# Kernel tuning notes

Hardware: AMD Instinct MI355X
Metric: run time of the kernel (lower is better)

Reference implementation:

```python
import jax, jax.numpy as jnp
import numpy as np

B, T, H, D = 16, 128, 512, 256
VIN, VOUT = 32000, 32000


def _lstm_cell(xt, h, c, W, U, b):
    # Keras LSTMCell gate order: i, f, g(candidate), o
    z = xt @ W + h @ U + b  # [B, 4H]
    i, f, g, o = jnp.split(z, 4, axis=-1)
    c = jax.nn.sigmoid(f) * c + jax.nn.sigmoid(i) * jnp.tanh(g)
    h = jax.nn.sigmoid(o) * jnp.tanh(c)
    return h, c


def _lstm_seq(x, W, U, b, h0, c0):
    # x: [B,T,Din] -> seq [B,T,H], final (h,c)
    def step(carry, xt):
        h, c = _lstm_cell(xt, carry[0], carry[1], W, U, b)
        return (h, c), h
    (hT, cT), seq = jax.lax.scan(step, (h0, c0), jnp.swapaxes(x, 0, 1))
    return jnp.swapaxes(seq, 0, 1), hT, cT


def setup_inputs() -> dict:
    key = jax.random.key(0)
    ks = jax.random.split(key, 16)
    s = lambda fan: 1.0 / np.sqrt(fan).astype(np.float32)
    f32 = jnp.float32
    return {
        "tokens": jax.random.randint(ks[0], (B, T), 0, VIN + 1),
        "emb": jax.random.normal(ks[1], (VIN + 1, D), f32) * 0.02,
        "W1": jax.random.normal(ks[2], (D, 4 * H), f32) * s(D),
        "U1": jax.random.normal(ks[3], (H, 4 * H), f32) * s(H),
        "b1": jnp.zeros((4 * H,), f32),
        "W2": jax.random.normal(ks[4], (H, 4 * H), f32) * s(H),
        "U2": jax.random.normal(ks[5], (H, 4 * H), f32) * s(H),
        "b2": jnp.zeros((4 * H,), f32),
        "Wd1": jax.random.normal(ks[6], (H, 4 * H), f32) * s(H),
        "Ud1": jax.random.normal(ks[7], (H, 4 * H), f32) * s(H),
        "bd1": jnp.zeros((4 * H,), f32),
        "Wd2": jax.random.normal(ks[8], (H, 4 * H), f32) * s(H),
        "Ud2": jax.random.normal(ks[9], (H, 4 * H), f32) * s(H),
        "bd2": jnp.zeros((4 * H,), f32),
        "Wo": jax.random.normal(ks[10], (2 * H, VOUT + 1), f32) * s(2 * H),
        "bo": jnp.zeros((VOUT + 1,), f32),
    }


def reference(tokens, emb, W1, U1, b1, W2, U2, b2, Wd1, Ud1, bd1, Wd2, Ud2, bd2, Wo, bo):
    x = emb[tokens]  # [B,T,D]
    zeros = jnp.zeros((tokens.shape[0], H), x.dtype)
    seq1, h1, c1 = _lstm_seq(x, W1, U1, b1, zeros, zeros)
    # layer-2 encoder initialized with layer-1 final states (as in source)
    seq2, h2, c2 = _lstm_seq(seq1, W2, U2, b2, h1, c1)

    def dec_step(carry, xt):
        (hA, cA), (hB, cB) = carry
        hA, cA = _lstm_cell(xt, hA, cA, Wd1, Ud1, bd1)
        hB, cB = _lstm_cell(hA, hB, cB, Wd2, Ud2, bd2)
        # global Luong dot attention over full encoder-2 sequence
        score = jax.nn.softmax(jnp.einsum('bsh,bh->bs', seq2, hB), axis=-1)
        ctx = jnp.einsum('bsh,bs->bh', seq2, score)
        out = jnp.concatenate([hB, ctx], axis=-1)  # [B, 2H]
        return ((hA, cA), (hB, cB)), out

    # decoder input is the encoder-2 sequence, time-major
    _, outs = jax.lax.scan(dec_step, ((h1, c1), (h2, c2)), jnp.swapaxes(seq2, 0, 1))
    dec = jnp.swapaxes(outs, 0, 1)  # [B,T,2H]
    logits = dec @ Wo + bo  # [B,T,VOUT+1]
    return jax.nn.softmax(logits, axis=-1)
```

## Files before the change

### kernel.cpp

```cpp
#include <hip/hip_runtime.h>
#include <hip/hip_bf16.h>
#include <math.h>

#define Bq   16
#define Tq   128
#define Hq   512
#define Dq   256
#define G4H  2048
#define MR   2048
#define VO   32001
#define NPAD 32128
#define NBLK 32
#define BH   (Bq * Hq)
#define HP64 4096

typedef unsigned int u32;
typedef unsigned long long u64;
typedef __attribute__((ext_vector_type(4))) float f32x4;
typedef __attribute__((ext_vector_type(8))) short bfrag;
typedef __attribute__((ext_vector_type(4))) float facc;

__device__ __forceinline__ float bf2f(short s) {
  union { unsigned u; float f; } v; v.u = ((unsigned)(unsigned short)s) << 16; return v.f;
}
__device__ __forceinline__ short f2bf(float f) {
  union { float f; unsigned u; } v; v.f = f;
  unsigned r = (v.u + 0x7fffu + ((v.u >> 16) & 1u)) >> 16;
  return (short)r;
}
__device__ __forceinline__ float sigm(float x) { return 1.0f / (1.0f + expf(-x)); }

__device__ __forceinline__ void ic_store64(u64* p, u64 v) {
  __hip_atomic_store(p, v, __ATOMIC_RELAXED, __HIP_MEMORY_SCOPE_AGENT);
}
__device__ __forceinline__ u64 ic_load64(const u64* p) {
  return __hip_atomic_load(p, __ATOMIC_RELAXED, __HIP_MEMORY_SCOPE_AGENT);
}

__device__ __forceinline__ void barsig(u32* flags, u32 ph) {
  asm volatile("s_waitcnt vmcnt(0)" ::: "memory");
  __syncthreads();
  if (threadIdx.x == 0)
    __hip_atomic_store(&flags[blockIdx.x * 32], ph, __ATOMIC_RELAXED, __HIP_MEMORY_SCOPE_AGENT);
}
__device__ __forceinline__ void barwait(u32* flags, u32 ph) {
  if (threadIdx.x < NBLK) {
    while (__hip_atomic_load(&flags[threadIdx.x * 32], __ATOMIC_RELAXED, __HIP_MEMORY_SCOPE_AGENT) < ph)
      __builtin_amdgcn_s_sleep(1);
  }
  __syncthreads();
}

__device__ __forceinline__ void* swz(void* plane, int row, int byteoff) {
  return (void*)((char*)plane + row * 1040 + (byteoff ^ ((row & 7) << 4)));
}

__global__ __launch_bounds__(256) void k_transcvt(const float* __restrict__ in,
                                                  short* __restrict__ out,
                                                  int R, int N, int perm) {
  __shared__ float tile[32][33];
  int nb = blockIdx.x * 32, rb = blockIdx.y * 32;
  int tx = threadIdx.x & 31, ty = threadIdx.x >> 5;
  for (int i = 0; i < 4; ++i) {
    int r = rb + ty + i * 8;
    int n = nb + tx;
    tile[ty + i * 8][tx] = (n < N) ? in[(size_t)r * N + n] : 0.0f;
  }
  __syncthreads();
  for (int i = 0; i < 4; ++i) {
    int n = nb + ty + i * 8;
    int orow = perm ? (((n & 511) << 2) | (n >> 9)) : n;
    out[(size_t)orow * R + rb + tx] = f2bf(tile[tx][ty + i * 8]);
  }
}

__global__ __launch_bounds__(256) void k_cvt(const float* __restrict__ in,
                                             short* __restrict__ out, int n) {
  int i = (blockIdx.x * 256 + threadIdx.x) * 4;
  if (i + 3 < n) {
    f32x4 v = *(const f32x4*)(in + i);
    short4 o;
    o.x = f2bf(v[0]); o.y = f2bf(v[1]); o.z = f2bf(v[2]); o.w = f2bf(v[3]);
    *(short4*)(out + i) = o;
  }
}

__global__ __launch_bounds__(256) void k_gather(const int* __restrict__ tokens,
                                                const float* __restrict__ emb,
                                                short* __restrict__ xbf) {
  int row = blockIdx.x;
  int t = row >> 4, b = row & 15;
  int tok = tokens[b * Tq + t];
  xbf[(size_t)row * Dq + threadIdx.x] = f2bf(emb[(size_t)tok * Dq + threadIdx.x]);
}

__global__ __launch_bounds__(256) void k_gemm(const short* __restrict__ A,
                                              const short* __restrict__ BT,
                                              float* __restrict__ C,
                                              const float* __restrict__ bias,
                                              int M, int Nreal, int K, int ldc,
                                              int permb) {
  __shared__ short lA[128 * 64];
  __shared__ short lB[128 * 64];
  const int tid = threadIdx.x;
  const int wave = tid >> 6, lane = tid & 63;
  const int l15 = lane & 15, l4 = lane >> 4;
  const int m0 = blockIdx.y * 128, n0 = blockIdx.x * 128;
  const int wm = (wave >> 1) * 64, wn = (wave & 1) * 64;
  facc acc[4][4] = {};

  for (int k0 = 0; k0 < K; k0 += 64) {
    __syncthreads();
    for (int i = 0; i < 4; ++i) {
      int c = i * 256 + wave * 64 + lane;
      int r = c >> 3, q = c & 7;
      int qs = q ^ (r & 7);
      const short* ga = A + (size_t)(m0 + r) * K + k0 + qs * 8;
      const short* gb = BT + (size_t)(n0 + r) * K + k0 + qs * 8;
      short* la = lA + (size_t)(i * 256 + wave * 64) * 8;
      short* lb = lB + (size_t)(i * 256 + wave * 64) * 8;
      __builtin_amdgcn_global_load_lds((const __attribute__((address_space(1))) u32*)ga,
                                       (__attribute__((address_space(3))) u32*)la, 16, 0, 0);
      __builtin_amdgcn_global_load_lds((const __attribute__((address_space(1))) u32*)gb,
                                       (__attribute__((address_space(3))) u32*)lb, 16, 0, 0);
    }
    __syncthreads();
    for (int ks = 0; ks < 2; ++ks) {
      bfrag a[4], b[4];
      for (int mi = 0; mi < 4; ++mi) {
        int r = wm + mi * 16 + l15;
        int qs = (ks * 4 + l4) ^ (r & 7);
        a[mi] = *(const bfrag*)&lA[r * 64 + qs * 8];
      }
      for (int ni = 0; ni < 4; ++ni) {
        int r = wn + ni * 16 + l15;
        int qs = (ks * 4 + l4) ^ (r & 7);
        b[ni] = *(const bfrag*)&lB[r * 64 + qs * 8];
      }
      for (int mi = 0; mi < 4; ++mi)
        for (int ni = 0; ni < 4; ++ni)
          acc[mi][ni] = __builtin_amdgcn_mfma_f32_16x16x32_bf16(a[mi], b[ni], acc[mi][ni], 0, 0, 0);
    }
  }
  for (int ni = 0; ni < 4; ++ni) {
    int col = n0 + wn + ni * 16 + l15;
    if (col >= Nreal) continue;
    int bcol = permb ? (((col & 3) << 9) | (col >> 2)) : col;
    float bs = bias ? bias[bcol] : 0.0f;
    for (int mi = 0; mi < 4; ++mi) {
      int rb = m0 + wm + mi * 16 + l4 * 4;
      facc v = acc[mi][ni];
      C[(size_t)(rb + 0) * ldc + col] = v[0] + bs;
      C[(size_t)(rb + 1) * ldc + col] = v[1] + bs;
      C[(size_t)(rb + 2) * ldc + col] = v[2] + bs;
      C[(size_t)(rb + 3) * ldc + col] = v[3] + bs;
    }
  }
}


__global__ __launch_bounds__(512) void k_rec(const float* __restrict__ XW,
                                             const short* __restrict__ UT,
                                             const float* __restrict__ hinit,
                                             const float* __restrict__ cinit,
                                             u64* __restrict__ hbuf,
                                             float* __restrict__ hfin,
                                             float* __restrict__ cfin,
                                             short* __restrict__ seq_bf,
                                             float* __restrict__ seq_f32,
                                             u32* flags, int dry) {
  __shared__ short lh[2][16][520];
  __shared__ float zt[8][16][20];
  const int tid = threadIdx.x;
  const int wv = tid >> 6, lane = tid & 63;
  const int l15 = lane & 15, l4 = lane >> 4;
  const int kh = wv >> 2;
  const int gw = blockIdx.x * 4 + (wv & 3);
  const int bb = lane >> 2, jj = lane & 3;
  const int hidx = gw * 4 + jj;

  bfrag ur[8];
  {
    const short* ub = UT + (size_t)(gw * 16 + l15) * Hq + kh * 256 + l4 * 8;
    #pragma unroll
    for (int ks = 0; ks < 8; ++ks) ur[ks] = *(const bfrag*)&ub[ks * 32];
  }
  float c = 0.0f;
  if (wv < 4) {
    c = cinit ? cinit[bb * Hq + hidx] : 0.0f;
    float hv = hinit ? hinit[bb * Hq + hidx] : 0.0f;
    int hi_ = (int)(unsigned short)f2bf(hv);
    int lo_ = (int)(unsigned short)f2bf(hv - bf2f((short)hi_));
    int hi2 = __shfl_xor(hi_, 1), lo2 = __shfl_xor(lo_, 1);
    if ((jj & 1) == 0) {
      u64 v = (u64)((u32)hi_ | ((u32)hi2 << 16)) | ((u64)((u32)lo_ | ((u32)lo2 << 16)) << 32);
      ic_store64(&hbuf[(bb * Hq + hidx) >> 1], v);
    }
  }
  u32 ph = 0;
  for (int d = 0; d < dry; ++d) { ++ph; barsig(flags, ph); barwait(flags, ph); }
  ++ph; barsig(flags, ph); barwait(flags, ph);

  for (int s = 0; s < Tq; ++s) {
    f32x4 xg = {};
    if (wv < 4) xg = *(const f32x4*)&XW[(size_t)(s * Bq + bb) * G4H + hidx * 4];
    const u64* hsrc = hbuf + (size_t)(s & 1) * HP64;
    #pragma unroll
    for (int it = 0; it < 8; ++it) {
      int i = it * 512 + tid;
      u64 v = ic_load64(&hsrc[i]);
      int b = i >> 8, bo = (i & 255) * 4;
      *(u32*)swz(&lh[0][0][0], b, bo) = (u32)v;
      *(u32*)swz(&lh[1][0][0], b, bo) = (u32)(v >> 32);
    }
    __syncthreads();
    facc a0 = {}, a1 = {};
    #pragma unroll
    for (int ks = 0; ks < 8; ++ks) {
      int bo = kh * 512 + ks * 64 + l4 * 16;
      bfrag ah = *(const bfrag*)swz(&lh[0][0][0], l15, bo);
      bfrag al = *(const bfrag*)swz(&lh[1][0][0], l15, bo);
      a0 = __builtin_amdgcn_mfma_f32_16x16x32_bf16(ah, ur[ks], a0, 0, 0, 0);
      a1 = __builtin_amdgcn_mfma_f32_16x16x32_bf16(al, ur[ks], a1, 0, 0, 0);
    }
    a0 += a1;
    *(f32x4*)&zt[wv][l15][l4 * 4] = a0;
    __syncthreads();
    float hN = 0.0f; int hi_ = 0;
    if (wv < 4) {
      float zi = zt[wv][4 * jj + 0][bb] + zt[wv + 4][4 * jj + 0][bb] + xg[0];
      float zf = zt[wv][4 * jj + 1][bb] + zt[wv + 4][4 * jj + 1][bb] + xg[1];
      float zg = zt[wv][4 * jj + 2][bb] + zt[wv + 4][4 * jj + 2][bb] + xg[2];
      float zo = zt[wv][4 * jj + 3][bb] + zt[wv + 4][4 * jj + 3][bb] + xg[3];
      c = sigm(zf) * c + sigm(zi) * tanhf(zg);
      hN = sigm(zo) * tanhf(c);
      hi_ = (int)(unsigned short)f2bf(hN);
      int lo_ = (int)(unsigned short)f2bf(hN - bf2f((short)hi_));
      int hi2 = __shfl_xor(hi_, 1), lo2 = __shfl_xor(lo_, 1);
      if (s < Tq - 1 && (jj & 1) == 0) {
        u64 v = (u64)((u32)hi_ | ((u32)hi2 << 16)) | ((u64)((u32)lo_ | ((u32)lo2 << 16)) << 32);
        ic_store64(&hbuf[(size_t)((s + 1) & 1) * HP64 + ((bb * Hq + hidx) >> 1)], v);
      }
    }
    if (s < Tq - 1) {
      ++ph; barsig(flags, ph);
      if (wv < 4) {
        seq_bf[(size_t)(s * Bq + bb) * Hq + hidx] = (short)hi_;
        if (seq_f32) seq_f32[(size_t)(s * Bq + bb) * Hq + hidx] = hN;
      }
      barwait(flags, ph);
    } else if (wv < 4) {
      seq_bf[(size_t)(s * Bq + bb) * Hq + hidx] = (short)hi_;
      if (seq_f32) seq_f32[(size_t)(s * Bq + bb) * Hq + hidx] = hN;
      hfin[bb * Hq + hidx] = hN;
      cfin[bb * Hq + hidx] = c;
    }
  }
}

__global__ __launch_bounds__(512) void k_dec2(const float* __restrict__ XW,
                                              const short* __restrict__ U1T,
                                              const short* __restrict__ W2T,
                                              const short* __restrict__ U2T,
                                              const float* __restrict__ bd2,
                                              const float* __restrict__ h1f, const float* __restrict__ c1f,
                                              const float* __restrict__ h2f, const float* __restrict__ c2f,
                                              u64* __restrict__ hAbuf, u64* __restrict__ hBbuf,
                                              float* __restrict__ hBseq, float* __restrict__ decb,
                                              u32* flags) {
  __shared__ short lA[2][16][520];
  __shared__ short lB[2][16][520];
  __shared__ float ztA[8][16][20];
  __shared__ float ztB[8][16][20];
  const int tid = threadIdx.x;
  const int wv = tid >> 6, lane = tid & 63;
  const int l15 = lane & 15, l4 = lane >> 4;
  const int kh = wv >> 2;
  const int gw = blockIdx.x * 4 + (wv & 3);
  const int bb = lane >> 2, jj = lane & 3;
  const int hidx = gw * 4 + jj;

  bfrag u1r[8], w2r[8], u2r[8];
  {
    size_t ro = (size_t)(gw * 16 + l15) * Hq + kh * 256 + l4 * 8;
    #pragma unroll
    for (int ks = 0; ks < 8; ++ks) {
      u1r[ks] = *(const bfrag*)&U1T[ro + ks * 32];
      w2r[ks] = *(const bfrag*)&W2T[ro + ks * 32];
      u2r[ks] = *(const bfrag*)&U2T[ro + ks * 32];
    }
  }
  float cc = 0.0f, bdi = 0, bdf = 0, bdg = 0, bdo = 0;
  {
    const float* cf = (wv < 4) ? c1f : c2f;
    const float* hf = (wv < 4) ? h1f : h2f;
    cc = cf[bb * Hq + hidx];
    float hv = hf[bb * Hq + hidx];
    int hi_ = (int)(unsigned short)f2bf(hv);
    int lo_ = (int)(unsigned short)f2bf(hv - bf2f((short)hi_));
    int hi2 = __shfl_xor(hi_, 1), lo2 = __shfl_xor(lo_, 1);
    if ((jj & 1) == 0) {
      u64 v = (u64)((u32)hi_ | ((u32)hi2 << 16)) | ((u64)((u32)lo_ | ((u32)lo2 << 16)) << 32);
      u64* hb = (wv < 4) ? hAbuf : hBbuf;
      int pi = (bb * Hq + hidx) >> 1;
      ic_store64(&hb[pi], v);
      ic_store64(&hb[HP64 + pi], v);
    }
    if (wv >= 4) {
      bdi = bd2[hidx]; bdf = bd2[Hq + hidx];
      bdg = bd2[2 * Hq + hidx]; bdo = bd2[3 * Hq + hidx];
    }
  }
  u32 ph = 1;
  barsig(flags, ph); barwait(flags, ph);

  for (int p = 0; p <= Tq; ++p) {
    f32x4 xg = {};
    if (wv < 4 && p < Tq) xg = *(const f32x4*)&XW[(size_t)(p * Bq + bb) * G4H + hidx * 4];
    const u64* asrc = hAbuf + (size_t)(p & 1) * HP64;
    const u64* bsrc = hBbuf + (size_t)(p & 1) * HP64;
    #pragma unroll
    for (int it = 0; it < 8; ++it) {
      int i = it * 512 + tid;
      u64 va = ic_load64(&asrc[i]);
      u64 vb = ic_load64(&bsrc[i]);
      int b = i >> 8, bo = (i & 255) * 4;
      *(u32*)swz(&lA[0][0][0], b, bo) = (u32)va;
      *(u32*)swz(&lA[1][0][0], b, bo) = (u32)(va >> 32);
      *(u32*)swz(&lB[0][0][0], b, bo) = (u32)vb;
      *(u32*)swz(&lB[1][0][0], b, bo) = (u32)(vb >> 32);
    }
    __syncthreads();

    facc a0 = {}, a1 = {}, b0 = {}, b1 = {}, b2 = {}, b3 = {};
    #pragma unroll
    for (int ks = 0; ks < 8; ++ks) {
      int bo = kh * 512 + ks * 64 + l4 * 16;
      bfrag ah = *(const bfrag*)swz(&lA[0][0][0], l15, bo);
      bfrag al = *(const bfrag*)swz(&lA[1][0][0], l15, bo);
      if (p < Tq) {
        a0 = __builtin_amdgcn_mfma_f32_16x16x32_bf16(ah, u1r[ks], a0, 0, 0, 0);
        a1 = __builtin_amdgcn_mfma_f32_16x16x32_bf16(al, u1r[ks], a1, 0, 0, 0);
      }
      if (p >= 1) {
        bfrag hh = *(const bfrag*)swz(&lB[0][0][0], l15, bo);
        bfrag hl = *(const bfrag*)swz(&lB[1][0][0], l15, bo);
        b0 = __builtin_amdgcn_mfma_f32_16x16x32_bf16(ah, w2r[ks], b0, 0, 0, 0);
        b1 = __builtin_amdgcn_mfma_f32_16x16x32_bf16(al, w2r[ks], b1, 0, 0, 0);
        b2 = __builtin_amdgcn_mfma_f32_16x16x32_bf16(hh, u2r[ks], b2, 0, 0, 0);
        b3 = __builtin_amdgcn_mfma_f32_16x16x32_bf16(hl, u2r[ks], b3, 0, 0, 0);
      }
    }
    if (p < Tq) { a0 += a1; *(f32x4*)&ztA[wv][l15][l4 * 4] = a0; }
    if (p >= 1) { b0 += b1; b0 += b2; b0 += b3; *(f32x4*)&ztB[wv][l15][l4 * 4] = b0; }
    __syncthreads();

    float hNB = 0.0f;
    if (wv < 4 && p < Tq) {
      float zi = ztA[wv][4 * jj + 0][bb] + ztA[wv + 4][4 * jj + 0][bb] + xg[0];
      float zf = ztA[wv][4 * jj + 1][bb] + ztA[wv + 4][4 * jj + 1][bb] + xg[1];
      float zg = ztA[wv][4 * jj + 2][bb] + ztA[wv + 4][4 * jj + 2][bb] + xg[2];
      float zo = ztA[wv][4 * jj + 3][bb] + ztA[wv + 4][4 * jj + 3][bb] + xg[3];
      cc = sigm(zf) * cc + sigm(zi) * tanhf(zg);
      float hN = sigm(zo) * tanhf(cc);
      int hi_ = (int)(unsigned short)f2bf(hN);
      int lo_ = (int)(unsigned short)f2bf(hN - bf2f((short)hi_));
      int hi2 = __shfl_xor(hi_, 1), lo2 = __shfl_xor(lo_, 1);
      if ((jj & 1) == 0) {
        u64 v = (u64)((u32)hi_ | ((u32)hi2 << 16)) | ((u64)((u32)lo_ | ((u32)lo2 << 16)) << 32);
        ic_store64(&hAbuf[(size_t)((p + 1) & 1) * HP64 + ((bb * Hq + hidx) >> 1)], v);
      }
    }
    if (wv >= 4 && p >= 1) {
      int pw = wv - 4;
      float zi = ztB[pw][4 * jj + 0][bb] + ztB[wv][4 * jj + 0][bb] + bdi;
      float zf = ztB[pw][4 * jj + 1][bb] + ztB[wv][4 * jj + 1][bb] + bdf;
      float zg = ztB[pw][4 * jj + 2][bb] + ztB[wv][4 * jj + 2][bb] + bdg;
      float zo = ztB[pw][4 * jj + 3][bb] + ztB[wv][4 * jj + 3][bb] + bdo;
      cc = sigm(zf) * cc + sigm(zi) * tanhf(zg);
      hNB = sigm(zo) * tanhf(cc);
      int hi_ = (int)(unsigned short)f2bf(hNB);
      int lo_ = (int)(unsigned short)f2bf(hNB - bf2f((short)hi_));
      int hi2 = __shfl_xor(hi_, 1), lo2 = __shfl_xor(lo_, 1);
      if (p < Tq && (jj & 1) == 0) {
        u64 v = (u64)((u32)hi_ | ((u32)hi2 << 16)) | ((u64)((u32)lo_ | ((u32)lo2 << 16)) << 32);
        ic_store64(&hBbuf[(size_t)((p + 1) & 1) * HP64 + ((bb * Hq + hidx) >> 1)], v);
      }
    }
    if (p < Tq) {
      ++ph; barsig(flags, ph);
      if (wv >= 4 && p >= 1) {
        int s = p - 1;
        hBseq[(size_t)(s * Bq + bb) * Hq + hidx] = hNB;
        decb[((size_t)bb * Tq + s) * (2 * Hq) + hidx] = hNB;
      }
      barwait(flags, ph);
    } else if (wv >= 4) {
      int s = Tq - 1;
      hBseq[(size_t)(s * Bq + bb) * Hq + hidx] = hNB;
      decb[((size_t)bb * Tq + s) * (2 * Hq) + hidx] = hNB;
    }
  }
}

__global__ __launch_bounds__(256) void k_attn(const float* __restrict__ seq2,
                                              const float* __restrict__ hBseq,
                                              float* __restrict__ dec) {
  int blk = blockIdx.x;
  int b = blk >> 7, t = blk & 127;
  __shared__ float q[Hq];
  __shared__ float part[256];
  __shared__ float p[Tq];
  int tid = threadIdx.x;
  const float* qsrc = hBseq + (size_t)(t * Bq + b) * Hq;
  q[tid] = qsrc[tid]; q[tid + 256] = qsrc[tid + 256];
  __syncthreads();
  {
    int s = tid >> 1, half = tid & 1;
    const float* row = seq2 + (size_t)(s * Bq + b) * Hq + half * 256;
    const float* qh = q + half * 256;
    float a = 0.0f;
    for (int k = 0; k < 256; k += 4) {
      f32x4 r4 = *(const f32x4*)(row + k);
      f32x4 q4 = *(const f32x4*)(qh + k);
      a += r4[0] * q4[0] + r4[1] * q4[1] + r4[2] * q4[2] + r4[3] * q4[3];
    }
    part[tid] = a;
  }
  __syncthreads();
  if (tid < 64) {
    float v0 = part[2 * tid] + part[2 * tid + 1];
    float v1 = part[2 * (tid + 64)] + part[2 * (tid + 64) + 1];
    float mx = fmaxf(v0, v1);
    for (int off = 32; off; off >>= 1) mx = fmaxf(mx, __shfl_xor(mx, off));
    float e0 = __expf(v0 - mx), e1 = __expf(v1 - mx);
    float sm = e0 + e1;
    for (int off = 32; off; off >>= 1) sm += __shfl_xor(sm, off);
    float inv = 1.0f / sm;
    p[tid] = e0 * inv; p[tid + 64] = e1 * inv;
  }
  __syncthreads();
  float c0 = 0.0f, c1 = 0.0f;
  for (int s = 0; s < Tq; ++s) {
    float ps = p[s];
    const float* row = seq2 + (size_t)(s * Bq + b) * Hq;
    c0 += ps * row[tid];
    c1 += ps * row[tid + 256];
  }
  float* drow = dec + (size_t)(b * Tq + t) * (2 * Hq) + Hq;
  drow[tid] = c0; drow[tid + 256] = c1;
}

__global__ __launch_bounds__(256) void k_softmax(float* __restrict__ L) {
  int row = blockIdx.x;
  float* p = L + (size_t)row * VO;
  int tid = threadIdx.x;
  float m = -3.0e38f, s = 0.0f;
  for (int i = tid; i < VO; i += 256) {
    float v = p[i];
    float mn = fmaxf(m, v);
    s = s * __expf(m - mn) + __expf(v - mn);
    m = mn;
  }
  __shared__ float sm[256], ss[256];
  sm[tid] = m; ss[tid] = s;
  __syncthreads();
  for (int off = 128; off; off >>= 1) {
    if (tid < off) {
      float m2 = sm[tid + off], s2 = ss[tid + off];
      float mn = fmaxf(sm[tid], m2);
      ss[tid] = ss[tid] * __expf(sm[tid] - mn) + s2 * __expf(m2 - mn);
      sm[tid] = mn;
    }
    __syncthreads();
  }
  float M = sm[0], IS = 1.0f / ss[0];
  for (int i = tid; i < VO; i += 256) {
    p[i] = __expf(p[i] - M) * IS;
  }
}

extern "C" void kernel_launch(void* const* d_in, const int* in_sizes, int n_in,
                              void* d_out, int out_size, void* d_ws, size_t ws_size,
                              hipStream_t stream) {
  const int*   tokens = (const int*)d_in[0];
  const float* emb    = (const float*)d_in[1];
  const float* W1     = (const float*)d_in[2];
  const float* U1     = (const float*)d_in[3];
  const float* b1     = (const float*)d_in[4];
  const float* W2     = (const float*)d_in[5];
  const float* U2     = (const float*)d_in[6];
  const float* b2     = (const float*)d_in[7];
  const float* Wd1    = (const float*)d_in[8];
  const float* Ud1    = (const float*)d_in[9];
  const float* bd1    = (const float*)d_in[10];
  const float* Wd2    = (const float*)d_in[11];
  const float* Ud2    = (const float*)d_in[12];
  const float* bd2    = (const float*)d_in[13];
  const float* Wo     = (const float*)d_in[14];
  const float* bo     = (const float*)d_in[15];
  float* out = (float*)d_out;

  size_t off = 0;
  char* base = (char*)d_ws;
  auto alloc = [&](size_t bytes) -> void* {
    void* p = base + off;
    off += (bytes + 255) & ~(size_t)255;
    return p;
  };
  u32*   flags   = (u32*)alloc(3 * 4096);
  short* x_bf    = (short*)alloc((size_t)MR * Dq * 2);
  short* W1T     = (short*)alloc((size_t)G4H * Dq * 2);
  short* W2T     = (short*)alloc((size_t)G4H * Hq * 2);
  short* Wd1T    = (short*)alloc((size_t)G4H * Hq * 2);
  short* WoT     = (short*)alloc((size_t)NPAD * (2 * Hq) * 2);
  short* U1T     = (short*)alloc((size_t)G4H * Hq * 2);
  short* U2T     = (short*)alloc((size_t)G4H * Hq * 2);
  short* Ud1T    = (short*)alloc((size_t)G4H * Hq * 2);
  short* Ud2T    = (short*)alloc((size_t)G4H * Hq * 2);
  short* Wd2T    = (short*)alloc((size_t)G4H * Hq * 2);
  float* XW      = (float*)alloc((size_t)MR * G4H * 4);
  short* seq1_bf = (short*)alloc((size_t)MR * Hq * 2);
  short* seq2_bf = (short*)alloc((size_t)MR * Hq * 2);
  float* seq2    = (float*)alloc((size_t)MR * Hq * 4);
  float* hBseq   = (float*)alloc((size_t)MR * Hq * 4);
  float* dec     = (float*)alloc((size_t)MR * 2 * Hq * 4);
  short* dec_bf  = (short*)alloc((size_t)MR * 2 * Hq * 2);
  u64*   h1buf   = (u64*)alloc((size_t)2 * HP64 * 8);
  u64*   h2buf   = (u64*)alloc((size_t)2 * HP64 * 8);
  u64*   hAbuf   = (u64*)alloc((size_t)2 * HP64 * 8);
  u64*   hBbuf   = (u64*)alloc((size_t)2 * HP64 * 8);
  float* h1f = (float*)alloc(BH * 4);
  float* c1f = (float*)alloc(BH * 4);
  float* h2f = (float*)alloc(BH * 4);
  float* c2f = (float*)alloc(BH * 4);
  u32* flags0 = flags;
  u32* flags1 = flags + 1024;
  u32* flags2 = flags + 2048;
  (void)ws_size; (void)in_sizes; (void)n_in; (void)out_size;

  hipMemsetAsync(flags, 0, 3 * 4096, stream);

  k_transcvt<<<dim3(G4H / 32, Dq / 32), 256, 0, stream>>>(W1, W1T, Dq, G4H, 1);
  k_transcvt<<<dim3(G4H / 32, Hq / 32), 256, 0, stream>>>(W2, W2T, Hq, G4H, 1);
  k_transcvt<<<dim3(G4H / 32, Hq / 32), 256, 0, stream>>>(Wd1, Wd1T, Hq, G4H, 1);
  k_transcvt<<<dim3(G4H / 32, Hq / 32), 256, 0, stream>>>(U1, U1T, Hq, G4H, 1);
  k_transcvt<<<dim3(G4H / 32, Hq / 32), 256, 0, stream>>>(U2, U2T, Hq, G4H, 1);
  k_transcvt<<<dim3(G4H / 32, Hq / 32), 256, 0, stream>>>(Ud1, Ud1T, Hq, G4H, 1);
  k_transcvt<<<dim3(G4H / 32, Hq / 32), 256, 0, stream>>>(Ud2, Ud2T, Hq, G4H, 1);
  k_transcvt<<<dim3(G4H / 32, Hq / 32), 256, 0, stream>>>(Wd2, Wd2T, Hq, G4H, 1);
  k_transcvt<<<dim3(NPAD / 32, (2 * Hq) / 32), 256, 0, stream>>>(Wo, WoT, 2 * Hq, VO, 0);

  k_gather<<<MR, 256, 0, stream>>>(tokens, emb, x_bf);

  k_gemm<<<dim3(G4H / 128, MR / 128), 256, 0, stream>>>(x_bf, W1T, XW, b1, MR, G4H, Dq, G4H, 1);
  k_rec<<<NBLK, 512, 0, stream>>>(XW, U1T, nullptr, nullptr, h1buf, h1f, c1f, seq1_bf, nullptr, flags0, 32);

  k_gemm<<<dim3(G4H / 128, MR / 128), 256, 0, stream>>>(seq1_bf, W2T, XW, b2, MR, G4H, Hq, G4H, 1);
  k_rec<<<NBLK, 512, 0, stream>>>(XW, U2T, h1f, c1f, h2buf, h2f, c2f, seq2_bf, seq2, flags1, 0);

  k_gemm<<<dim3(G4H / 128, MR / 128), 256, 0, stream>>>(seq2_bf, Wd1T, XW, bd1, MR, G4H, Hq, G4H, 1);
  k_dec2<<<NBLK, 512, 0, stream>>>(XW, Ud1T, Wd2T, Ud2T, bd2, h1f, c1f, h2f, c2f,
                                   hAbuf, hBbuf, hBseq, dec, flags2);

  k_attn<<<MR, 256, 0, stream>>>(seq2, hBseq, dec);
  k_cvt<<<(MR * 2 * Hq) / 1024, 256, 0, stream>>>(dec, dec_bf, MR * 2 * Hq);
  k_gemm<<<dim3(NPAD / 128, MR / 128), 256, 0, stream>>>(dec_bf, WoT, out, bo, MR, VO, 2 * Hq, VO, 0);
  k_softmax<<<MR, 256, 0, stream>>>(out);
}
```

Baseline: 2.814 ms.

## Replace grid flag barriers with sentinel-filled per-step hidden-state dataflow buffers

Each recurrence step now writes its hidden state into its own slot of a large buffer that is pre-filled with a NaN sentinel. Consumers spin on the data itself until no sentinel remains, which removes the two-phase flag barrier per timestep and the dry-run barrier warmup. Attention now reads bf16 sequence and query data and writes bf16 output directly, so the fp32 seq2, hBseq and dec buffers and the separate conversion kernel are gone. The trade-offs are a large sentinel fill at startup and a deadlock if a real bf16 value ever equals the sentinel pattern. Attention accuracy is also reduced by using bf16 operands.

```diff
diff --git a/kernel.cpp b/kernel.cpp
--- a/kernel.cpp
+++ b/kernel.cpp
@@ -12,7 +12,8 @@
 #define NPAD 32128
 #define NBLK 32
 #define BH   (Bq * Hq)
-#define HP64 4096
+#define SENTW 0x7FC0u
+#define SENT64 0x7FC07FC07FC07FC0ull
 
 typedef unsigned int u32;
 typedef unsigned long long u64;
@@ -28,6 +29,9 @@
   unsigned r = (v.u + 0x7fffu + ((v.u >> 16) & 1u)) >> 16;
   return (short)r;
 }
+__device__ __forceinline__ float asf(u32 u) {
+  union { u32 u; float f; } v; v.u = u; return v.f;
+}
 __device__ __forceinline__ float sigm(float x) { return 1.0f / (1.0f + expf(-x)); }
 
 __device__ __forceinline__ void ic_store64(u64* p, u64 v) {
@@ -37,22 +41,13 @@
   return __hip_atomic_load(p, __ATOMIC_RELAXED, __HIP_MEMORY_SCOPE_AGENT);
 }
 
-__device__ __forceinline__ void barsig(u32* flags, u32 ph) {
-  asm volatile("s_waitcnt vmcnt(0)" ::: "memory");
-  __syncthreads();
-  if (threadIdx.x == 0)
-    __hip_atomic_store(&flags[blockIdx.x * 32], ph, __ATOMIC_RELAXED, __HIP_MEMORY_SCOPE_AGENT);
-}
-__device__ __forceinline__ void barwait(u32* flags, u32 ph) {
-  if (threadIdx.x < NBLK) {
-    while (__hip_atomic_load(&flags[threadIdx.x * 32], __ATOMIC_RELAXED, __HIP_MEMORY_SCOPE_AGENT) < ph)
-      __builtin_amdgcn_s_sleep(1);
-  }
-  __syncthreads();
-}
-
 __device__ __forceinline__ void* swz(void* plane, int row, int byteoff) {
   return (void*)((char*)plane + row * 1040 + (byteoff ^ ((row & 7) << 4)));
+}
+
+__global__ __launch_bounds__(256) void k_fill(u64* __restrict__ p, int n) {
+  int i = blockIdx.x * 256 + threadIdx.x;
+  if (i < n) p[i] = SENT64;
 }
 
 __global__ __launch_bounds__(256) void k_transcvt(const float* __restrict__ in,
@@ -71,17 +66,6 @@
     int n = nb + ty + i * 8;
     int orow = perm ? (((n & 511) << 2) | (n >> 9)) : n;
     out[(size_t)orow * R + rb + tx] = f2bf(tile[tx][ty + i * 8]);
-  }
-}
-
-__global__ __launch_bounds__(256) void k_cvt(const float* __restrict__ in,
-                                             short* __restrict__ out, int n) {
-  int i = (blockIdx.x * 256 + threadIdx.x) * 4;
-  if (i + 3 < n) {
-    f32x4 v = *(const f32x4*)(in + i);
-    short4 o;
-    o.x = f2bf(v[0]); o.y = f2bf(v[1]); o.z = f2bf(v[2]); o.w = f2bf(v[3]);
-    *(short4*)(out + i) = o;
   }
 }
 
@@ -159,16 +143,14 @@
 }
 
 
-__global__ __launch_bounds__(512) void k_rec(const float* __restrict__ XW,
-                                             const short* __restrict__ UT,
-                                             const float* __restrict__ hinit,
-                                             const float* __restrict__ cinit,
-                                             u64* __restrict__ hbuf,
-                                             float* __restrict__ hfin,
-                                             float* __restrict__ cfin,
-                                             short* __restrict__ seq_bf,
-                                             float* __restrict__ seq_f32,
-                                             u32* flags, int dry) {
+__global__ __launch_bounds__(512, 1) void k_rec(const float* __restrict__ XW,
+                                                const short* __restrict__ UT,
+                                                const float* __restrict__ hinit,
+                                                const float* __restrict__ cinit,
+                                                u64* __restrict__ hbuf,
+                                                float* __restrict__ hfin,
+                                                float* __restrict__ cfin,
+                                                short* __restrict__ seq_bf) {
   __shared__ short lh[2][16][520];
   __shared__ float zt[8][16][20];
   const int tid = threadIdx.x;
@@ -197,21 +179,27 @@
       ic_store64(&hbuf[(bb * Hq + hidx) >> 1], v);
     }
   }
-  u32 ph = 0;
-  for (int d = 0; d < dry; ++d) { ++ph; barsig(flags, ph); barwait(flags, ph); }
-  ++ph; barsig(flags, ph); barwait(flags, ph);
 
   for (int s = 0; s < Tq; ++s) {
     f32x4 xg = {};
     if (wv < 4) xg = *(const f32x4*)&XW[(size_t)(s * Bq + bb) * G4H + hidx * 4];
-    const u64* hsrc = hbuf + (size_t)(s & 1) * HP64;
+    const u64* hsrc = hbuf + (size_t)s * 4096;
+    u64 v[8];
+    for (;;) {
+      #pragma unroll
+      for (int it = 0; it < 8; ++it) v[it] = ic_load64(&hsrc[it * 512 + tid]);
+      u32 bad = 0;
+      #pragma unroll
+      for (int it = 0; it < 8; ++it) bad |= (((u32)v[it] & 0xFFFFu) == SENTW);
+      if (!bad) break;
+      __builtin_amdgcn_s_sleep(1);
+    }
     #pragma unroll
     for (int it = 0; it < 8; ++it) {
       int i = it * 512 + tid;
-      u64 v = ic_load64(&hsrc[i]);
       int b = i >> 8, bo = (i & 255) * 4;
-      *(u32*)swz(&lh[0][0][0], b, bo) = (u32)v;
-      *(u32*)swz(&lh[1][0][0], b, bo) = (u32)(v >> 32);
+      *(u32*)swz(&lh[0][0][0], b, bo) = (u32)v[it];
+      *(u32*)swz(&lh[1][0][0], b, bo) = (u32)(v[it] >> 32);
     }
     __syncthreads();
     facc a0 = {}, a1 = {};
@@ -226,48 +214,35 @@
     a0 += a1;
     *(f32x4*)&zt[wv][l15][l4 * 4] = a0;
     __syncthreads();
-    float hN = 0.0f; int hi_ = 0;
     if (wv < 4) {
       float zi = zt[wv][4 * jj + 0][bb] + zt[wv + 4][4 * jj + 0][bb] + xg[0];
       float zf = zt[wv][4 * jj + 1][bb] + zt[wv + 4][4 * jj + 1][bb] + xg[1];
       float zg = zt[wv][4 * jj + 2][bb] + zt[wv + 4][4 * jj + 2][bb] + xg[2];
       float zo = zt[wv][4 * jj + 3][bb] + zt[wv + 4][4 * jj + 3][bb] + xg[3];
       c = sigm(zf) * c + sigm(zi) * tanhf(zg);
-      hN = sigm(zo) * tanhf(c);
-      hi_ = (int)(unsigned short)f2bf(hN);
+      float hN = sigm(zo) * tanhf(c);
+      int hi_ = (int)(unsigned short)f2bf(hN);
       int lo_ = (int)(unsigned short)f2bf(hN - bf2f((short)hi_));
       int hi2 = __shfl_xor(hi_, 1), lo2 = __shfl_xor(lo_, 1);
       if (s < Tq - 1 && (jj & 1) == 0) {
-        u64 v = (u64)((u32)hi_ | ((u32)hi2 << 16)) | ((u64)((u32)lo_ | ((u32)lo2 << 16)) << 32);
-        ic_store64(&hbuf[(size_t)((s + 1) & 1) * HP64 + ((bb * Hq + hidx) >> 1)], v);
-      }
-    }
-    if (s < Tq - 1) {
-      ++ph; barsig(flags, ph);
-      if (wv < 4) {
-        seq_bf[(size_t)(s * Bq + bb) * Hq + hidx] = (short)hi_;
-        if (seq_f32) seq_f32[(size_t)(s * Bq + bb) * Hq + hidx] = hN;
-      }
-      barwait(flags, ph);
-    } else if (wv < 4) {
+        u64 v2 = (u64)((u32)hi_ | ((u32)hi2 << 16)) | ((u64)((u32)lo_ | ((u32)lo2 << 16)) << 32);
+        ic_store64(&hbuf[(size_t)(s + 1) * 4096 + ((bb * Hq + hidx) >> 1)], v2);
+      }
       seq_bf[(size_t)(s * Bq + bb) * Hq + hidx] = (short)hi_;
-      if (seq_f32) seq_f32[(size_t)(s * Bq + bb) * Hq + hidx] = hN;
-      hfin[bb * Hq + hidx] = hN;
-      cfin[bb * Hq + hidx] = c;
-    }
-  }
-}
-
-__global__ __launch_bounds__(512) void k_dec2(const float* __restrict__ XW,
-                                              const short* __restrict__ U1T,
-                                              const short* __restrict__ W2T,
-                                              const short* __restrict__ U2T,
-                                              const float* __restrict__ bd2,
-                                              const float* __restrict__ h1f, const float* __restrict__ c1f,
-                                              const float* __restrict__ h2f, const float* __restrict__ c2f,
-                                              u64* __restrict__ hAbuf, u64* __restrict__ hBbuf,
-                                              float* __restrict__ hBseq, float* __restrict__ decb,
-                                              u32* flags) {
+      if (s == Tq - 1) { hfin[bb * Hq + hidx] = hN; cfin[bb * Hq + hidx] = c; }
+    }
+  }
+}
+
+__global__ __launch_bounds__(512, 1) void k_dec2(const float* __restrict__ XW,
+                                                 const short* __restrict__ U1T,
+                                                 const short* __restrict__ W2T,
+                                                 const short* __restrict__ U2T,
+                                                 const float* __restrict__ bd2,
+                                                 const float* __restrict__ h1f, const float* __restrict__ c1f,
+                                                 const float* __restrict__ h2f, const float* __restrict__ c2f,
+                                                 u64* __restrict__ hAbuf, u64* __restrict__ hBbuf,
+                                                 short* __restrict__ hBseq_bf, short* __restrict__ dec_bf) {
   __shared__ short lA[2][16][520];
   __shared__ short lB[2][16][520];
   __shared__ float ztA[8][16][20];
@@ -301,34 +276,49 @@
     int hi2 = __shfl_xor(hi_, 1), lo2 = __shfl_xor(lo_, 1);
     if ((jj & 1) == 0) {
       u64 v = (u64)((u32)hi_ | ((u32)hi2 << 16)) | ((u64)((u32)lo_ | ((u32)lo2 << 16)) << 32);
-      u64* hb = (wv < 4) ? hAbuf : hBbuf;
       int pi = (bb * Hq + hidx) >> 1;
-      ic_store64(&hb[pi], v);
-      ic_store64(&hb[HP64 + pi], v);
+      if (wv < 4) {
+        ic_store64(&hAbuf[pi], v);
+      } else {
+        ic_store64(&hBbuf[pi], v);
+        ic_store64(&hBbuf[4096 + pi], v);
+      }
     }
     if (wv >= 4) {
       bdi = bd2[hidx]; bdf = bd2[Hq + hidx];
       bdg = bd2[2 * Hq + hidx]; bdo = bd2[3 * Hq + hidx];
     }
   }
-  u32 ph = 1;
-  barsig(flags, ph); barwait(flags, ph);
 
   for (int p = 0; p <= Tq; ++p) {
     f32x4 xg = {};
     if (wv < 4 && p < Tq) xg = *(const f32x4*)&XW[(size_t)(p * Bq + bb) * G4H + hidx * 4];
-    const u64* asrc = hAbuf + (size_t)(p & 1) * HP64;
-    const u64* bsrc = hBbuf + (size_t)(p & 1) * HP64;
+    const u64* asrc = hAbuf + (size_t)p * 4096;
+    const u64* bsrc = hBbuf + (size_t)p * 4096;
+    u64 va[8], vb[8];
+    for (;;) {
+      #pragma unroll
+      for (int it = 0; it < 8; ++it) {
+        va[it] = ic_load64(&asrc[it * 512 + tid]);
+        vb[it] = ic_load64(&bsrc[it * 512 + tid]);
+      }
+      u32 bad = 0;
+      #pragma unroll
+      for (int it = 0; it < 8; ++it) {
+        bad |= (((u32)va[it] & 0xFFFFu) == SENTW);
+        bad |= (((u32)vb[it] & 0xFFFFu) == SENTW);
+      }
+      if (!bad) break;
+      __builtin_amdgcn_s_sleep(1);
+    }
     #pragma unroll
     for (int it = 0; it < 8; ++it) {
       int i = it * 512 + tid;
-      u64 va = ic_load64(&asrc[i]);
-      u64 vb = ic_load64(&bsrc[i]);
       int b = i >> 8, bo = (i & 255) * 4;
-      *(u32*)swz(&lA[0][0][0], b, bo) = (u32)va;
-      *(u32*)swz(&lA[1][0][0], b, bo) = (u32)(va >> 32);
-      *(u32*)swz(&lB[0][0][0], b, bo) = (u32)vb;
-      *(u32*)swz(&lB[1][0][0], b, bo) = (u32)(vb >> 32);
+      *(u32*)swz(&lA[0][0][0], b, bo) = (u32)va[it];
+      *(u32*)swz(&lA[1][0][0], b, bo) = (u32)(va[it] >> 32);
+      *(u32*)swz(&lB[0][0][0], b, bo) = (u32)vb[it];
+      *(u32*)swz(&lB[1][0][0], b, bo) = (u32)(vb[it] >> 32);
     }
     __syncthreads();
 
@@ -355,7 +345,6 @@
     if (p >= 1) { b0 += b1; b0 += b2; b0 += b3; *(f32x4*)&ztB[wv][l15][l4 * 4] = b0; }
     __syncthreads();
 
-    float hNB = 0.0f;
     if (wv < 4 && p < Tq) {
       float zi = ztA[wv][4 * jj + 0][bb] + ztA[wv + 4][4 * jj + 0][bb] + xg[0];
       float zf = ztA[wv][4 * jj + 1][bb] + ztA[wv + 4][4 * jj + 1][bb] + xg[1];
@@ -368,62 +357,51 @@
       int hi2 = __shfl_xor(hi_, 1), lo2 = __shfl_xor(lo_, 1);
       if ((jj & 1) == 0) {
         u64 v = (u64)((u32)hi_ | ((u32)hi2 << 16)) | ((u64)((u32)lo_ | ((u32)lo2 << 16)) << 32);
-        ic_store64(&hAbuf[(size_t)((p + 1) & 1) * HP64 + ((bb * Hq + hidx) >> 1)], v);
+        ic_store64(&hAbuf[(size_t)(p + 1) * 4096 + ((bb * Hq + hidx) >> 1)], v);
       }
     }
     if (wv >= 4 && p >= 1) {
+      int s = p - 1;
       int pw = wv - 4;
       float zi = ztB[pw][4 * jj + 0][bb] + ztB[wv][4 * jj + 0][bb] + bdi;
       float zf = ztB[pw][4 * jj + 1][bb] + ztB[wv][4 * jj + 1][bb] + bdf;
       float zg = ztB[pw][4 * jj + 2][bb] + ztB[wv][4 * jj + 2][bb] + bdg;
       float zo = ztB[pw][4 * jj + 3][bb] + ztB[wv][4 * jj + 3][bb] + bdo;
       cc = sigm(zf) * cc + sigm(zi) * tanhf(zg);
-      hNB = sigm(zo) * tanhf(cc);
-      int hi_ = (int)(unsigned short)f2bf(hNB);
-      int lo_ = (int)(unsigned short)f2bf(hNB - bf2f((short)hi_));
+      float hN = sigm(zo) * tanhf(cc);
+      int hi_ = (int)(unsigned short)f2bf(hN);
+      int lo_ = (int)(unsigned short)f2bf(hN - bf2f((short)hi_));
       int hi2 = __shfl_xor(hi_, 1), lo2 = __shfl_xor(lo_, 1);
       if (p < Tq && (jj & 1) == 0) {
         u64 v = (u64)((u32)hi_ | ((u32)hi2 << 16)) | ((u64)((u32)lo_ | ((u32)lo2 << 16)) << 32);
-        ic_store64(&hBbuf[(size_t)((p + 1) & 1) * HP64 + ((bb * Hq + hidx) >> 1)], v);
-      }
-    }
-    if (p < Tq) {
-      ++ph; barsig(flags, ph);
-      if (wv >= 4 && p >= 1) {
-        int s = p - 1;
-        hBseq[(size_t)(s * Bq + bb) * Hq + hidx] = hNB;
-        decb[((size_t)bb * Tq + s) * (2 * Hq) + hidx] = hNB;
-      }
-      barwait(flags, ph);
-    } else if (wv >= 4) {
-      int s = Tq - 1;
-      hBseq[(size_t)(s * Bq + bb) * Hq + hidx] = hNB;
-      decb[((size_t)bb * Tq + s) * (2 * Hq) + hidx] = hNB;
-    }
-  }
-}
-
-__global__ __launch_bounds__(256) void k_attn(const float* __restrict__ seq2,
-                                              const float* __restrict__ hBseq,
-                                              float* __restrict__ dec) {
+        ic_store64(&hBbuf[(size_t)(p + 1) * 4096 + ((bb * Hq + hidx) >> 1)], v);
+      }
+      hBseq_bf[(size_t)(s * Bq + bb) * Hq + hidx] = (short)hi_;
+      dec_bf[((size_t)bb * Tq + s) * (2 * Hq) + hidx] = (short)hi_;
+    }
+  }
+}
+
+__global__ __launch_bounds__(256) void k_attn(const short* __restrict__ seq2b,
+                                              const short* __restrict__ hqb,
+                                              short* __restrict__ decb) {
   int blk = blockIdx.x;
   int b = blk >> 7, t = blk & 127;
-  __shared__ float q[Hq];
+  __shared__ u32 q[256];
   __shared__ float part[256];
   __shared__ float p[Tq];
   int tid = threadIdx.x;
-  const float* qsrc = hBseq + (size_t)(t * Bq + b) * Hq;
-  q[tid] = qsrc[tid]; q[tid + 256] = qsrc[tid + 256];
+  q[tid] = *(const u32*)&hqb[(size_t)(t * Bq + b) * Hq + tid * 2];
   __syncthreads();
   {
     int s = tid >> 1, half = tid & 1;
-    const float* row = seq2 + (size_t)(s * Bq + b) * Hq + half * 256;
-    const float* qh = q + half * 256;
+    const u32* row = (const u32*)&seq2b[(size_t)(s * Bq + b) * Hq + half * 256];
+    const u32* qh = q + half * 128;
     float a = 0.0f;
-    for (int k = 0; k < 256; k += 4) {
-      f32x4 r4 = *(const f32x4*)(row + k);
-      f32x4 q4 = *(const f32x4*)(qh + k);
-      a += r4[0] * q4[0] + r4[1] * q4[1] + r4[2] * q4[2] + r4[3] * q4[3];
+    #pragma unroll 8
+    for (int k = 0; k < 128; ++k) {
+      u32 r = row[k], qq = qh[k];
+      a += asf(r << 16) * asf(qq << 16) + asf(r & 0xFFFF0000u) * asf(qq & 0xFFFF0000u);
     }
     part[tid] = a;
   }
@@ -443,12 +421,12 @@
   float c0 = 0.0f, c1 = 0.0f;
   for (int s = 0; s < Tq; ++s) {
     float ps = p[s];
-    const float* row = seq2 + (size_t)(s * Bq + b) * Hq;
-    c0 += ps * row[tid];
-    c1 += ps * row[tid + 256];
-  }
-  float* drow = dec + (size_t)(b * Tq + t) * (2 * Hq) + Hq;
-  drow[tid] = c0; drow[tid + 256] = c1;
+    u32 r = *(const u32*)&seq2b[(size_t)(s * Bq + b) * Hq + tid * 2];
+    c0 += ps * asf(r << 16);
+    c1 += ps * asf(r & 0xFFFF0000u);
+  }
+  u32 o = ((u32)(unsigned short)f2bf(c0)) | (((u32)(unsigned short)f2bf(c1)) << 16);
+  *(u32*)&decb[(size_t)(b * Tq + t) * (2 * Hq) + Hq + tid * 2] = o;
 }
 
 __global__ __launch_bounds__(256) void k_softmax(float* __restrict__ L) {
@@ -508,7 +486,6 @@
     off += (bytes + 255) & ~(size_t)255;
     return p;
   };
-  u32*   flags   = (u32*)alloc(3 * 4096);
   short* x_bf    = (short*)alloc((size_t)MR * Dq * 2);
   short* W1T     = (short*)alloc((size_t)G4H * Dq * 2);
   short* W2T     = (short*)alloc((size_t)G4H * Hq * 2);
@@ -522,24 +499,23 @@
   float* XW      = (float*)alloc((size_t)MR * G4H * 4);
   short* seq1_bf = (short*)alloc((size_t)MR * Hq * 2);
   short* seq2_bf = (short*)alloc((size_t)MR * Hq * 2);
-  float* seq2    = (float*)alloc((size_t)MR * Hq * 4);
-  float* hBseq   = (float*)alloc((size_t)MR * Hq * 4);
-  float* dec     = (float*)alloc((size_t)MR * 2 * Hq * 4);
+  short* hBseqbf = (short*)alloc((size_t)MR * Hq * 2);
   short* dec_bf  = (short*)alloc((size_t)MR * 2 * Hq * 2);
-  u64*   h1buf   = (u64*)alloc((size_t)2 * HP64 * 8);
-  u64*   h2buf   = (u64*)alloc((size_t)2 * HP64 * 8);
-  u64*   hAbuf   = (u64*)alloc((size_t)2 * HP64 * 8);
-  u64*   hBbuf   = (u64*)alloc((size_t)2 * HP64 * 8);
+  u64*   hflow   = (u64*)alloc((size_t)514 * 4096 * 8);
+  u64*   h1buf   = hflow;
+  u64*   h2buf   = hflow + (size_t)128 * 4096;
+  u64*   hAbuf   = hflow + (size_t)256 * 4096;
+  u64*   hBbuf   = hflow + (size_t)385 * 4096;
   float* h1f = (float*)alloc(BH * 4);
   float* c1f = (float*)alloc(BH * 4);
   float* h2f = (float*)alloc(BH * 4);
   float* c2f = (float*)alloc(BH * 4);
-  u32* flags0 = flags;
-  u32* flags1 = flags + 1024;
-  u32* flags2 = flags + 2048;
   (void)ws_size; (void)in_sizes; (void)n_in; (void)out_size;
 
-  hipMemsetAsync(flags, 0, 3 * 4096, stream);
+  {
+    int n = 514 * 4096;
+    k_fill<<<(n + 255) / 256, 256, 0, stream>>>(hflow, n);
+  }
 
   k_transcvt<<<dim3(G4H / 32, Dq / 32), 256, 0, stream>>>(W1, W1T, Dq, G4H, 1);
   k_transcvt<<<dim3(G4H / 32, Hq / 32), 256, 0, stream>>>(W2, W2T, Hq, G4H, 1);
@@ -554,17 +530,16 @@
   k_gather<<<MR, 256, 0, stream>>>(tokens, emb, x_bf);
 
   k_gemm<<<dim3(G4H / 128, MR / 128), 256, 0, stream>>>(x_bf, W1T, XW, b1, MR, G4H, Dq, G4H, 1);
-  k_rec<<<NBLK, 512, 0, stream>>>(XW, U1T, nullptr, nullptr, h1buf, h1f, c1f, seq1_bf, nullptr, flags0, 32);
+  k_rec<<<NBLK, 512, 0, stream>>>(XW, U1T, nullptr, nullptr, h1buf, h1f, c1f, seq1_bf);
 
   k_gemm<<<dim3(G4H / 128, MR / 128), 256, 0, stream>>>(seq1_bf, W2T, XW, b2, MR, G4H, Hq, G4H, 1);
-  k_rec<<<NBLK, 512, 0, stream>>>(XW, U2T, h1f, c1f, h2buf, h2f, c2f, seq2_bf, seq2, flags1, 0);
+  k_rec<<<NBLK, 512, 0, stream>>>(XW, U2T, h1f, c1f, h2buf, h2f, c2f, seq2_bf);
 
   k_gemm<<<dim3(G4H / 128, MR / 128), 256, 0, stream>>>(seq2_bf, Wd1T, XW, bd1, MR, G4H, Hq, G4H, 1);
   k_dec2<<<NBLK, 512, 0, stream>>>(XW, Ud1T, Wd2T, Ud2T, bd2, h1f, c1f, h2f, c2f,
-                                   hAbuf, hBbuf, hBseq, dec, flags2);
-
-  k_attn<<<MR, 256, 0, stream>>>(seq2, hBseq, dec);
-  k_cvt<<<(MR * 2 * Hq) / 1024, 256, 0, stream>>>(dec, dec_bf, MR * 2 * Hq);
+                                   hAbuf, hBbuf, hBseqbf, dec_bf);
+
+  k_attn<<<MR, 256, 0, stream>>>(seq2_bf, hBseqbf, dec_bf);
   k_gemm<<<dim3(NPAD / 128, MR / 128), 256, 0, stream>>>(dec_bf, WoT, out, bo, MR, VO, 2 * Hq, VO, 0);
   k_softmax<<<MR, 256, 0, stream>>>(out);
 }
```

New measurement: 2.311 ms. 17.9% less time.
